# Optimization experiments

Hardware: AMD Instinct MI355X
Metric: run time of the kernel (lower is better)

## Reference

```python
import jax, jax.numpy as jnp
import numpy as np


def _top2_margin(logits, targets):
    # logits: [N, C], targets: [N] int
    top2, _ = jax.lax.top_k(logits, 2)                       # [N, 2]
    tgt_logit = jnp.take_along_axis(logits, targets[:, None], axis=1)[:, 0]  # [N]
    # margin = top1 - top2 if the target class attains the max, else 0
    return jnp.where(tgt_logit == top2[:, 0], top2[:, 0] - top2[:, 1],
                     jnp.zeros((), dtype=logits.dtype))


def setup_inputs() -> dict:
    key = jax.random.key(0)
    ks = jax.random.split(key, 6)
    N, C = 16384, 1000
    return {
        "outputs1": jax.random.normal(ks[0], (N, C), dtype=jnp.float32),
        "outputs2": jax.random.normal(ks[1], (N, C), dtype=jnp.float32),
        "outputs3": jax.random.normal(ks[2], (N, C), dtype=jnp.float32),
        "outputs4": jax.random.normal(ks[3], (N, C), dtype=jnp.float32),
        "mimic": jax.random.normal(ks[4], (N, C), dtype=jnp.float32),
        "targets": jax.random.randint(ks[5], (N,), 0, C, dtype=jnp.int64),
        "n_test": N,
    }


def reference(outputs1, outputs2, outputs3, outputs4, mimic, targets, n_test):
    T = 2.0  # temperature (init kwarg)
    # n_test == N; the loop over samples is fully vectorized here.
    margins = jnp.stack([
        _top2_margin(outputs1, targets),
        _top2_margin(outputs2, targets),
        _top2_margin(outputs3, targets),
        _top2_margin(outputs4, targets),
        _top2_margin(mimic, targets),
    ], axis=1)                                               # [N, 5]
    out_threshold = jax.nn.softmax(margins / T, axis=1)      # [N, 5]
    max_preds = jnp.maximum(jnp.maximum(outputs1.max(), outputs2.max()),
                            jnp.maximum(outputs3.max(), outputs4.max()))
    return (max_preds, out_threshold)
```

## Files before the change

kernel.cpp:

```cpp
#include <hip/hip_runtime.h>
#include <math.h>

#define NROWS 16384
#define NCOLS 1000
#define NMAT  5
#define WPB   4
#define BLOCKS_A (NROWS / WPB)

__global__ __launch_bounds__(256) void fused_kernel(
    const float* __restrict__ o0, const float* __restrict__ o1,
    const float* __restrict__ o2, const float* __restrict__ o3,
    const float* __restrict__ o4, const int* __restrict__ targets,
    float* __restrict__ out, float* __restrict__ blockmax)
{
    const int wave = threadIdx.x >> 6;
    const int lane = threadIdx.x & 63;
    const int row  = blockIdx.x * WPB + wave;

    const float* rows[NMAT];
    rows[0] = o0 + (size_t)row * NCOLS;
    rows[1] = o1 + (size_t)row * NCOLS;
    rows[2] = o2 + (size_t)row * NCOLS;
    rows[3] = o3 + (size_t)row * NCOLS;
    rows[4] = o4 + (size_t)row * NCOLS;

    float4 v[NMAT][4];
    #pragma unroll
    for (int m = 0; m < NMAT; ++m) {
        const float4* b = (const float4*)rows[m];
        v[m][0] = b[lane];
        v[m][1] = b[lane + 64];
        v[m][2] = b[lane + 128];
        v[m][3] = make_float4(-INFINITY, -INFINITY, -INFINITY, -INFINITY);
    }
    if (lane < 58) {
        #pragma unroll
        for (int m = 0; m < NMAT; ++m)
            v[m][3] = ((const float4*)rows[m])[lane + 192];
    }

    float t1[NMAT], t2[NMAT];
#define UPD(m, x) { float _mn = fminf(t1[m], (x)); t1[m] = fmaxf(t1[m], (x)); \
                    t2[m] = fmaxf(t2[m], _mn); }
    #pragma unroll
    for (int m = 0; m < NMAT; ++m) {
        t1[m] = -INFINITY; t2[m] = -INFINITY;
        #pragma unroll
        for (int q = 0; q < 4; ++q) {
            UPD(m, v[m][q].x) UPD(m, v[m][q].y)
            UPD(m, v[m][q].z) UPD(m, v[m][q].w)
        }
    }
#undef UPD

    #pragma unroll
    for (int off = 32; off > 0; off >>= 1) {
        float a1[NMAT], a2[NMAT];
        #pragma unroll
        for (int m = 0; m < NMAT; ++m) {
            a1[m] = __shfl_xor(t1[m], off);
            a2[m] = __shfl_xor(t2[m], off);
        }
        #pragma unroll
        for (int m = 0; m < NMAT; ++m) {
            float mn = fminf(t1[m], a1[m]);
            t1[m] = fmaxf(t1[m], a1[m]);
            t2[m] = fmaxf(fmaxf(t2[m], a2[m]), mn);
        }
    }

    if (lane == 0) {
        const int t = targets[row];
        float mg[NMAT];
        #pragma unroll
        for (int m = 0; m < NMAT; ++m) {
            const float tgt = rows[m][t];
            mg[m] = (tgt == t1[m]) ? (t1[m] - t2[m]) : 0.0f;
        }
        float mx = mg[0];
        #pragma unroll
        for (int m = 1; m < NMAT; ++m) mx = fmaxf(mx, mg[m]);
        float e[NMAT], s = 0.0f;
        #pragma unroll
        for (int m = 0; m < NMAT; ++m) { e[m] = __expf((mg[m] - mx) * 0.5f); s += e[m]; }
        const float inv = 1.0f / s;
        #pragma unroll
        for (int m = 0; m < NMAT; ++m) out[1 + row * NMAT + m] = e[m] * inv;
    }

    __shared__ float smax[WPB];
    if (lane == 0)
        smax[wave] = fmaxf(fmaxf(t1[0], t1[1]), fmaxf(t1[2], t1[3]));
    __syncthreads();
    if (threadIdx.x == 0)
        blockmax[blockIdx.x] =
            fmaxf(fmaxf(smax[0], smax[1]), fmaxf(smax[2], smax[3]));
}

__global__ __launch_bounds__(256) void reduce_kernel(
    const float* __restrict__ blockmax, float* __restrict__ out)
{
    __shared__ float red[256];
    float mm = -INFINITY;
    for (int k = threadIdx.x; k < BLOCKS_A; k += 256)
        mm = fmaxf(mm, blockmax[k]);
    red[threadIdx.x] = mm;
    __syncthreads();
    #pragma unroll
    for (int s = 128; s > 0; s >>= 1) {
        if (threadIdx.x < s)
            red[threadIdx.x] = fmaxf(red[threadIdx.x], red[threadIdx.x + s]);
        __syncthreads();
    }
    if (threadIdx.x == 0) out[0] = red[0];
}

extern "C" void kernel_launch(void* const* d_in, const int* in_sizes, int n_in,
                              void* d_out, int out_size, void* d_ws, size_t ws_size,
                              hipStream_t stream) {
    const float* o0 = (const float*)d_in[0];
    const float* o1 = (const float*)d_in[1];
    const float* o2 = (const float*)d_in[2];
    const float* o3 = (const float*)d_in[3];
    const float* o4 = (const float*)d_in[4];
    const int*   tg = (const int*)d_in[5];
    float* out = (float*)d_out;

    float* blockmax = (float*)d_ws;

    fused_kernel<<<BLOCKS_A, 256, 0, stream>>>(o0, o1, o2, o3, o4, tg,
                                               out, blockmax);
    reduce_kernel<<<1, 256, 0, stream>>>(blockmax, out);
}
```

Measured before the change: 296.0 us.

## Split per-matrix top-2 across grid y dimension and move softmax to separate kernel

The fused kernel, where each wave handled one row across all five matrices, is split so that each block in grid.y handles a single matrix. This cuts register pressure and multiplies the number of blocks five-fold. The target logit is now taken from registers with a wave shuffle instead of a separate global load. The softmax over the five margins moves into a new small kernel that reads the margins back from the output buffer, adding one launch and an extra global round trip. The max reduction now covers four times as many block maxima.

```diff
diff --git a/kernel.cpp b/kernel.cpp
--- a/kernel.cpp
+++ b/kernel.cpp
@@ -5,9 +5,9 @@
 #define NCOLS 1000
 #define NMAT  5
 #define WPB   4
-#define BLOCKS_A (NROWS / WPB)
+#define GRIDX (NROWS / WPB)
 
-__global__ __launch_bounds__(256) void fused_kernel(
+__global__ __launch_bounds__(256) void topk_kernel(
     const float* __restrict__ o0, const float* __restrict__ o1,
     const float* __restrict__ o2, const float* __restrict__ o3,
     const float* __restrict__ o4, const int* __restrict__ targets,
@@ -16,93 +16,80 @@
     const int wave = threadIdx.x >> 6;
     const int lane = threadIdx.x & 63;
     const int row  = blockIdx.x * WPB + wave;
+    const int m    = blockIdx.y;
 
-    const float* rows[NMAT];
-    rows[0] = o0 + (size_t)row * NCOLS;
-    rows[1] = o1 + (size_t)row * NCOLS;
-    rows[2] = o2 + (size_t)row * NCOLS;
-    rows[3] = o3 + (size_t)row * NCOLS;
-    rows[4] = o4 + (size_t)row * NCOLS;
+    const float* base = (m == 0) ? o0 : (m == 1) ? o1 : (m == 2) ? o2
+                      : (m == 3) ? o3 : o4;
+    const float4* b = (const float4*)(base + (size_t)row * NCOLS);
 
-    float4 v[NMAT][4];
-    #pragma unroll
-    for (int m = 0; m < NMAT; ++m) {
-        const float4* b = (const float4*)rows[m];
-        v[m][0] = b[lane];
-        v[m][1] = b[lane + 64];
-        v[m][2] = b[lane + 128];
-        v[m][3] = make_float4(-INFINITY, -INFINITY, -INFINITY, -INFINITY);
-    }
-    if (lane < 58) {
-        #pragma unroll
-        for (int m = 0; m < NMAT; ++m)
-            v[m][3] = ((const float4*)rows[m])[lane + 192];
-    }
+    const int t = targets[row];
 
-    float t1[NMAT], t2[NMAT];
-#define UPD(m, x) { float _mn = fminf(t1[m], (x)); t1[m] = fmaxf(t1[m], (x)); \
-                    t2[m] = fmaxf(t2[m], _mn); }
-    #pragma unroll
-    for (int m = 0; m < NMAT; ++m) {
-        t1[m] = -INFINITY; t2[m] = -INFINITY;
-        #pragma unroll
-        for (int q = 0; q < 4; ++q) {
-            UPD(m, v[m][q].x) UPD(m, v[m][q].y)
-            UPD(m, v[m][q].z) UPD(m, v[m][q].w)
-        }
-    }
+    float4 v0 = b[lane];
+    float4 v1 = b[lane + 64];
+    float4 v2 = b[lane + 128];
+    float4 v3 = (lane < 58) ? b[lane + 192]
+                            : make_float4(-INFINITY, -INFINITY, -INFINITY, -INFINITY);
+
+    float t1 = -INFINITY, t2 = -INFINITY;
+#define UPD(x) { float _mn = fminf(t1, (x)); t1 = fmaxf(t1, (x)); \
+                 t2 = fmaxf(t2, _mn); }
+    UPD(v0.x) UPD(v0.y) UPD(v0.z) UPD(v0.w)
+    UPD(v1.x) UPD(v1.y) UPD(v1.z) UPD(v1.w)
+    UPD(v2.x) UPD(v2.y) UPD(v2.z) UPD(v2.w)
+    UPD(v3.x) UPD(v3.y) UPD(v3.z) UPD(v3.w)
 #undef UPD
+
+    const int q = t >> 2, comp = t & 3, src = q & 63, chunk = q >> 6;
+    float4 cv = (chunk == 0) ? v0 : (chunk == 1) ? v1 : (chunk == 2) ? v2 : v3;
+    float cand = (comp == 0) ? cv.x : (comp == 1) ? cv.y
+               : (comp == 2) ? cv.z : cv.w;
+    const float tv = __shfl(cand, src);
 
     #pragma unroll
     for (int off = 32; off > 0; off >>= 1) {
-        float a1[NMAT], a2[NMAT];
-        #pragma unroll
-        for (int m = 0; m < NMAT; ++m) {
-            a1[m] = __shfl_xor(t1[m], off);
-            a2[m] = __shfl_xor(t2[m], off);
-        }
-        #pragma unroll
-        for (int m = 0; m < NMAT; ++m) {
-            float mn = fminf(t1[m], a1[m]);
-            t1[m] = fmaxf(t1[m], a1[m]);
-            t2[m] = fmaxf(fmaxf(t2[m], a2[m]), mn);
-        }
+        float a1 = __shfl_xor(t1, off);
+        float a2 = __shfl_xor(t2, off);
+        float mn = fminf(t1, a1);
+        t1 = fmaxf(t1, a1);
+        t2 = fmaxf(fmaxf(t2, a2), mn);
     }
 
-    if (lane == 0) {
-        const int t = targets[row];
-        float mg[NMAT];
-        #pragma unroll
-        for (int m = 0; m < NMAT; ++m) {
-            const float tgt = rows[m][t];
-            mg[m] = (tgt == t1[m]) ? (t1[m] - t2[m]) : 0.0f;
-        }
-        float mx = mg[0];
-        #pragma unroll
-        for (int m = 1; m < NMAT; ++m) mx = fmaxf(mx, mg[m]);
-        float e[NMAT], s = 0.0f;
-        #pragma unroll
-        for (int m = 0; m < NMAT; ++m) { e[m] = __expf((mg[m] - mx) * 0.5f); s += e[m]; }
-        const float inv = 1.0f / s;
-        #pragma unroll
-        for (int m = 0; m < NMAT; ++m) out[1 + row * NMAT + m] = e[m] * inv;
+    if (lane == 0)
+        out[1 + row * NMAT + m] = (tv == t1) ? (t1 - t2) : 0.0f;
+
+    if (m < 4) {
+        __shared__ float smax[WPB];
+        if (lane == 0) smax[wave] = t1;
+        __syncthreads();
+        if (threadIdx.x == 0)
+            blockmax[m * GRIDX + blockIdx.x] =
+                fmaxf(fmaxf(smax[0], smax[1]), fmaxf(smax[2], smax[3]));
     }
-
-    __shared__ float smax[WPB];
-    if (lane == 0)
-        smax[wave] = fmaxf(fmaxf(t1[0], t1[1]), fmaxf(t1[2], t1[3]));
-    __syncthreads();
-    if (threadIdx.x == 0)
-        blockmax[blockIdx.x] =
-            fmaxf(fmaxf(smax[0], smax[1]), fmaxf(smax[2], smax[3]));
 }
 
-__global__ __launch_bounds__(256) void reduce_kernel(
+__global__ __launch_bounds__(256) void softmax_kernel(float* __restrict__ out)
+{
+    const int i = blockIdx.x * 256 + threadIdx.x;
+    float mg[NMAT];
+    #pragma unroll
+    for (int m = 0; m < NMAT; ++m) mg[m] = out[1 + i * NMAT + m];
+    float mx = mg[0];
+    #pragma unroll
+    for (int m = 1; m < NMAT; ++m) mx = fmaxf(mx, mg[m]);
+    float e[NMAT], s = 0.0f;
+    #pragma unroll
+    for (int m = 0; m < NMAT; ++m) { e[m] = __expf((mg[m] - mx) * 0.5f); s += e[m]; }
+    const float inv = 1.0f / s;
+    #pragma unroll
+    for (int m = 0; m < NMAT; ++m) out[1 + i * NMAT + m] = e[m] * inv;
+}
+
+__global__ __launch_bounds__(256) void max_kernel(
     const float* __restrict__ blockmax, float* __restrict__ out)
 {
     __shared__ float red[256];
     float mm = -INFINITY;
-    for (int k = threadIdx.x; k < BLOCKS_A; k += 256)
+    for (int k = threadIdx.x; k < 4 * GRIDX; k += 256)
         mm = fmaxf(mm, blockmax[k]);
     red[threadIdx.x] = mm;
     __syncthreads();
@@ -128,7 +115,8 @@
 
     float* blockmax = (float*)d_ws;
 
-    fused_kernel<<<BLOCKS_A, 256, 0, stream>>>(o0, o1, o2, o3, o4, tg,
-                                               out, blockmax);
-    reduce_kernel<<<1, 256, 0, stream>>>(blockmax, out);
+    topk_kernel<<<dim3(GRIDX, NMAT), 256, 0, stream>>>(
+        o0, o1, o2, o3, o4, tg, out, blockmax);
+    softmax_kernel<<<NROWS / 256, 256, 0, stream>>>(out);
+    max_kernel<<<1, 256, 0, stream>>>(blockmax, out);
 }
```

Measured after the change: 301.5 us. Within noise of the previous version (+1.9%).
